# Kernel optimization log

Hardware: AMD Instinct MI355X
Metric: run time of the kernel (lower is better)

## Reference

```python
import jax, jax.numpy as jnp
import numpy as np

N, CH, H, W = 2, 64, 96, 96
NH, CHUNK, RED = 4, 144, 4
CM = CH // RED  # match channels = 16
RES_SCALE = 1.0
NORM_EPS = 5e-5


def conv2d(x, w, b):
    # 3x3 'same' conv, NCHW / OIHW
    y = jax.lax.conv_general_dilated(x, w, (1, 1), 'SAME',
                                     dimension_numbers=('NCHW', 'OIHW', 'NCHW'))
    return y + b[None, :, None, None]


def setup_inputs() -> dict:
    key = jax.random.key(0)
    ks = jax.random.split(key, 8)
    L = H * W
    hb = min(L // CHUNK + (L // CHUNK) % 2, 128)  # = 64
    x = jax.random.normal(ks[0], (N, CH, H, W), jnp.float32)
    # per-round semi-orthogonal rotations: rows of (CM, hb) orthonormal
    g = jax.random.normal(ks[1], (NH, hb, CM), jnp.float32)
    q = jnp.stack([jnp.linalg.qr(g[h])[0] for h in range(NH)])  # (NH, hb, CM)
    rot = jnp.transpose(q, (2, 0, 1))  # (CM, NH, hb)
    def s(k, shape, fan):
        return jax.random.normal(k, shape, jnp.float32) / np.sqrt(fan).astype(np.float32)
    wm = s(ks[2], (CM, CH, 3, 3), CH * 9)
    wa = s(ks[3], (CH, CH, 3, 3), CH * 9)
    wf = s(ks[4], (CH, CH, 3, 3), CH * 9)
    fc1_w = s(ks[5], (CHUNK, CH), CH)
    fc2_w = s(ks[6], (CHUNK, CHUNK), CHUNK)
    return {'x': x, 'rot': rot,
            'wm': wm, 'bm': jnp.zeros((CM,), jnp.float32),
            'wa': wa, 'ba': jnp.zeros((CH,), jnp.float32),
            'wf': wf, 'bf': jnp.zeros((CH,), jnp.float32),
            'fc1_w': fc1_w, 'fc1_b': jnp.zeros((CHUNK,), jnp.float32),
            'fc2_w': fc2_w, 'fc2_b': jnp.zeros((CHUNK,), jnp.float32)}


def reference(x, rot, wm, bm, wa, ba, wf, bf, fc1_w, fc1_b, fc2_w, fc2_b):
    n, _, h, w = x.shape
    L = h * w
    hb = rot.shape[-1]
    # embeddings: (N, L, C)
    xe = jax.nn.relu(conv2d(x, wm, bm)).reshape(n, CM, L).transpose(0, 2, 1)
    ye = jax.nn.relu(conv2d(x, wa, ba)).reshape(n, CH, L).transpose(0, 2, 1)
    fe = jax.nn.relu(conv2d(x, wf, bf)).reshape(n, CH, L).transpose(0, 2, 1)
    # LSH: argmax over rotated directions, offset per round (detached in original)
    rv = jnp.einsum('ntf,fhi->nhti', xe, rot)  # (N, NH, L, hb)
    codes = jnp.argmax(rv, -1) + (jnp.arange(NH) * hb)[None, :, None]
    codes = codes.reshape(n, NH * L)
    idx = jnp.argsort(codes, axis=-1)
    undo = jnp.argsort(idx, axis=-1)
    mod = idx % L
    gather = lambda t: jnp.take_along_axis(t, mod[..., None], axis=1)
    nch = L // CHUNK  # L chosen divisible by CHUNK -> padding = 0
    xs = gather(xe).reshape(n, NH, nch, CHUNK, CM)
    ys = gather(ye).reshape(n, NH, nch, CHUNK, CH)
    fs = gather(fe).reshape(n, NH, nch, CHUNK, CH)
    nrm = jnp.linalg.norm(xs, axis=-1, keepdims=True)
    xmatch = xs / jnp.maximum(nrm, NORM_EPS)
    adj = lambda t: jnp.concatenate([t, jnp.roll(t, 1, axis=2), jnp.roll(t, -1, axis=2)], axis=3)
    xmatch = adj(xmatch)   # (n, NH, nch, 3*CHUNK, CM)
    ya = adj(ys)           # (n, NH, nch, 3*CHUNK, CH)
    fa = adj(fs)           # (n, NH, nch, 3*CHUNK, CH)
    hid = jax.nn.relu(fa @ fc1_w.T + fc1_b)
    fc_raw = jnp.swapaxes(hid @ fc2_w.T + fc2_b, -1, -2)  # (n, NH, nch, CHUNK, 3*CHUNK)
    raw = jnp.einsum('nhkie,nhkje->nhkij', xs, xmatch) + fc_raw
    bsc = jax.scipy.special.logsumexp(raw, axis=-1, keepdims=True)
    score = jnp.exp(raw - bsc)
    ret = jnp.einsum('nhkij,nhkje->nhkie', score, ya)  # (n, NH, nch, CHUNK, CH)
    ret = ret.reshape(n, NH * L, CH)
    bsc = bsc.reshape(n, NH * L)
    ret = jnp.take_along_axis(ret, undo[..., None], axis=1)
    bsc = jnp.take_along_axis(bsc, undo, axis=1)
    ret = ret.reshape(n, NH, L, CH)
    probs = jax.nn.softmax(bsc.reshape(n, NH, L, 1), axis=1)
    out = jnp.sum(ret * probs, axis=1)  # (n, L, CH)
    out = out.transpose(0, 2, 1).reshape(n, CH, h, w)
    return out * RES_SCALE + x
```

## Files before the change

kernel.cpp:

```cpp
#include <hip/hip_runtime.h>
#include <hip/hip_bf16.h>

#define LL 9216
#define TOT 36864
#define CHK 144
#define NSEG 144
#define EPS_N 5e-5f

typedef __bf16 bf16x8 __attribute__((ext_vector_type(8)));
typedef float f32x4 __attribute__((ext_vector_type(4)));

__device__ __forceinline__ float dot4(float4 a, float4 b) {
    return a.x*b.x + a.y*b.y + a.z*b.z + a.w*b.w;
}
__device__ __forceinline__ unsigned short f2bf(float f) {
    __hip_bfloat16 h = __float2bfloat16(f);
    return *reinterpret_cast<unsigned short*>(&h);
}
__device__ __forceinline__ float bf2f(unsigned short u) {
    return __uint_as_float(((unsigned int)u) << 16);
}

__global__ __launch_bounds__(256) void k_front(
    const float* __restrict__ x, const float* __restrict__ wm,
    const float* __restrict__ bm, const float* __restrict__ rot,
    unsigned short* __restrict__ xeb, unsigned short* __restrict__ xnb,
    unsigned char* __restrict__ codes,
    const float* __restrict__ fc1w, const float* __restrict__ fc2w,
    const float* __restrict__ wa, const float* __restrict__ wf,
    unsigned short* __restrict__ w1bf, unsigned short* __restrict__ w2bf,
    unsigned short* __restrict__ wpack)
{
    int tid = threadIdx.x;
    if (blockIdx.x >= 288) {
        int i = (blockIdx.x - 288) * 256 + tid;
        if (i < 144 * 64) w1bf[i] = f2bf(fc1w[i]);
        if (i < 144 * 160) {
            int r = i / 160, c = i - r * 160;
            w2bf[i] = (c < 144) ? f2bf(fc2w[r * 144 + c]) : 0;
        }
        if (i < 128 * 576) {
            int o = i / 576, kk = i - o * 576;
            int dydx = kk >> 6, c = kk & 63;
            const float* src = (o < 64) ? wa : wf;
            wpack[i] = f2bf(src[(o & 63) * 576 + c * 9 + dydx]);
        }
        return;
    }
    __shared__ float xl[6400];
    __shared__ float rotT[4096];
    __shared__ float xsp[64 * 20];
    int b = blockIdx.x;
    int n = b / 144, tile = b % 144;
    int ty0 = (tile / 12) * 8, tx0 = (tile % 12) * 8;
    for (int li = tid; li < 6400; li += 256) {
        int c = li / 100, s = li % 100;
        int yy = s / 10, xx = s % 10;
        int gy = ty0 + yy - 1, gx = tx0 + xx - 1;
        float v = 0.f;
        if ((unsigned)gy < 96u && (unsigned)gx < 96u)
            v = x[((n * 64 + c) * 96 + gy) * 96 + gx];
        xl[li] = v;
    }
    for (int e = tid; e < 4096; e += 256) {
        int f = e >> 8, r = e & 255;
        rotT[r * 16 + f] = rot[f * 256 + r];
    }
    __syncthreads();
    int p = tid & 63, og = tid >> 6;
    int row = p >> 3, col = p & 7;
    int ogs = __builtin_amdgcn_readfirstlane(og);
    const float* wb = wm + (size_t)ogs * 4 * 576;
    float acc0 = 0.f, acc1 = 0.f, acc2 = 0.f, acc3 = 0.f;
    for (int c = 0; c < 64; ++c) {
        float xp[9];
        int base = c * 100 + row * 10 + col;
        #pragma unroll
        for (int dy = 0; dy < 3; ++dy)
            #pragma unroll
            for (int dx = 0; dx < 3; ++dx)
                xp[dy * 3 + dx] = xl[base + dy * 10 + dx];
        const float* w0 = wb + c * 9;
        #pragma unroll
        for (int u = 0; u < 9; ++u) {
            acc0 += w0[u]        * xp[u];
            acc1 += w0[576 + u]  * xp[u];
            acc2 += w0[1152 + u] * xp[u];
            acc3 += w0[1728 + u] * xp[u];
        }
    }
    int o = ogs * 4;
    float v0 = acc0 + bm[o + 0]; v0 = v0 > 0.f ? v0 : 0.f;
    float v1 = acc1 + bm[o + 1]; v1 = v1 > 0.f ? v1 : 0.f;
    float v2 = acc2 + bm[o + 2]; v2 = v2 > 0.f ? v2 : 0.f;
    float v3 = acc3 + bm[o + 3]; v3 = v3 > 0.f ? v3 : 0.f;
    size_t t = (size_t)n * LL + (ty0 + row) * 96 + tx0 + col;
    unsigned short pk[4] = {f2bf(v0), f2bf(v1), f2bf(v2), f2bf(v3)};
    *(uint2*)(xeb + t * 16 + o) = *(uint2*)pk;
    *(float4*)(xsp + p * 20 + o) = make_float4(v0, v1, v2, v3);
    __syncthreads();
    int pos = tid & 63, h = tid >> 6;
    int prow = pos >> 3, pcol = pos & 7;
    size_t tc = (size_t)n * LL + (ty0 + prow) * 96 + tx0 + pcol;
    float4 q0 = *(float4*)(xsp + pos * 20 + 0);
    float4 q1 = *(float4*)(xsp + pos * 20 + 4);
    float4 q2 = *(float4*)(xsp + pos * 20 + 8);
    float4 q3 = *(float4*)(xsp + pos * 20 + 12);
    if (h == 0) {
        float nn = dot4(q0,q0) + dot4(q1,q1) + dot4(q2,q2) + dot4(q3,q3);
        float s = fmaxf(sqrtf(nn), EPS_N);
        float inv = 1.f / s;
        unsigned short pn[16];
        pn[0]=f2bf(q0.x*inv);  pn[1]=f2bf(q0.y*inv);  pn[2]=f2bf(q0.z*inv);  pn[3]=f2bf(q0.w*inv);
        pn[4]=f2bf(q1.x*inv);  pn[5]=f2bf(q1.y*inv);  pn[6]=f2bf(q1.z*inv);  pn[7]=f2bf(q1.w*inv);
        pn[8]=f2bf(q2.x*inv);  pn[9]=f2bf(q2.y*inv);  pn[10]=f2bf(q2.z*inv); pn[11]=f2bf(q2.w*inv);
        pn[12]=f2bf(q3.x*inv); pn[13]=f2bf(q3.y*inv); pn[14]=f2bf(q3.z*inv); pn[15]=f2bf(q3.w*inv);
        *(uint4*)(xnb + tc * 16)     = ((uint4*)pn)[0];
        *(uint4*)(xnb + tc * 16 + 8) = ((uint4*)pn)[1];
    }
    float best = -1e30f; int bi = 0;
    const float* rp = rotT + h * 1024;
    for (int i = 0; i < 64; ++i) {
        const float4* r4 = (const float4*)(rp + i * 16);
        float v = dot4(q0, r4[0]) + dot4(q1, r4[1]) + dot4(q2, r4[2]) + dot4(q3, r4[3]);
        if (v > best) { best = v; bi = i; }
    }
    codes[(size_t)n * TOT + h * LL + (tc - (size_t)n * LL)] = (unsigned char)(h * 64 + bi);
}

__global__ __launch_bounds__(256) void k_convbf_fc(
    const float* __restrict__ x, const unsigned short* __restrict__ wpack,
    const float* __restrict__ ba, const float* __restrict__ bfb,
    const unsigned short* __restrict__ w1bf, const float* __restrict__ fc1_b,
    const unsigned short* __restrict__ w2bf, const float* __restrict__ fc2_b,
    unsigned short* __restrict__ yeb, unsigned short* __restrict__ re2b,
    const unsigned char* __restrict__ codes, int* __restrict__ hist)
{
    __shared__ unsigned short xt[3 * 50 * 72];
    __shared__ unsigned short fet[48 * 72];
    __shared__ unsigned short hb [48 * 168];
    __shared__ int lh[256];
    int tid = threadIdx.x;
    if (blockIdx.x >= 384) {
        int b2 = blockIdx.x - 384;
        int n = b2 / NSEG, seg = b2 % NSEG;
        lh[tid] = 0;
        __syncthreads();
        int code = codes[(size_t)n * TOT + seg * 256 + tid];
        atomicAdd(&lh[code], 1);
        __syncthreads();
        hist[((size_t)n * 256 + tid) * NSEG + seg] = lh[tid];
        return;
    }
    int b = blockIdx.x;
    int n = b / 192, rem = b % 192;
    int y = rem >> 1, strip = rem & 1;
    int x0 = strip * 48;
    for (int e = tid; e < 9600; e += 256) {
        int r = e / 3200, r2 = e - r * 3200;
        int c = r2 / 50, j = r2 - c * 50;
        int gy = y - 1 + r, gx = x0 - 1 + j;
        float v = 0.f;
        if ((unsigned)gy < 96u && (unsigned)gx < 96u)
            v = x[((n * 64 + c) * 96 + gy) * 96 + gx];
        xt[(r * 50 + j) * 72 + c] = f2bf(v);
    }
    for (int e = tid; e < 384; e += 256) {
        int r = e >> 3, pq = e & 7;
        *(unsigned int*)(hb + r * 168 + 144 + pq * 2) = 0;
    }
    __syncthreads();
    int wave = tid >> 6, lane = tid & 63;
    int n16 = lane & 15, quad = lane >> 4;
    f32x4 acc[2][3];
    #pragma unroll
    for (int mi = 0; mi < 2; ++mi)
        #pragma unroll
        for (int nt = 0; nt < 3; ++nt) acc[mi][nt] = (f32x4){0.f, 0.f, 0.f, 0.f};
    #pragma unroll
    for (int s = 0; s < 18; ++s) {
        int dydx = s >> 1, half = s & 1;
        int dy = dydx / 3, dxm = dydx - dy * 3;
        bf16x8 B[3];
        #pragma unroll
        for (int nt = 0; nt < 3; ++nt) {
            int j = nt * 16 + n16 + dxm;
            B[nt] = *(bf16x8*)(xt + (dy * 50 + j) * 72 + half * 32 + quad * 8);
        }
        #pragma unroll
        for (int mi = 0; mi < 2; ++mi) {
            int o = (wave * 2 + mi) * 16 + n16;
            bf16x8 A = *(const bf16x8*)(wpack + o * 576 + dydx * 64 + half * 32 + quad * 8);
            #pragma unroll
            for (int nt = 0; nt < 3; ++nt)
                acc[mi][nt] = __builtin_amdgcn_mfma_f32_16x16x32_bf16(A, B[nt], acc[mi][nt], 0, 0, 0);
        }
    }
    #pragma unroll
    for (int mi = 0; mi < 2; ++mi) {
        int mt = wave * 2 + mi;
        int obase = mt * 16 + quad * 4;
        float4 b4 = (mt < 4) ? *(const float4*)(ba + obase)
                             : *(const float4*)(bfb + obase - 64);
        #pragma unroll
        for (int nt = 0; nt < 3; ++nt) {
            int j = nt * 16 + n16;
            unsigned short pk[4];
            float v0 = acc[mi][nt][0] + b4.x; pk[0] = f2bf(v0 > 0.f ? v0 : 0.f);
            float v1 = acc[mi][nt][1] + b4.y; pk[1] = f2bf(v1 > 0.f ? v1 : 0.f);
            float v2 = acc[mi][nt][2] + b4.z; pk[2] = f2bf(v2 > 0.f ? v2 : 0.f);
            float v3 = acc[mi][nt][3] + b4.w; pk[3] = f2bf(v3 > 0.f ? v3 : 0.f);
            if (mt < 4) {
                size_t t = (size_t)n * LL + y * 96 + x0 + j;
                *(uint2*)(yeb + t * 64 + obase) = *(uint2*)pk;
            } else {
                *(uint2*)(fet + j * 72 + (obase - 64)) = *(uint2*)pk;
            }
        }
    }
    __syncthreads();
    size_t R0 = (size_t)n * LL + y * 96 + x0;
    for (int nt = wave; nt < 9; nt += 4) {
        int bn = nt * 16 + n16;
        bf16x8 b0 = *(const bf16x8*)(w1bf + bn * 64 + quad * 8);
        bf16x8 b1 = *(const bf16x8*)(w1bf + bn * 64 + 32 + quad * 8);
        float bb = fc1_b[bn];
        #pragma unroll
        for (int m = 0; m < 3; ++m) {
            int arow = m * 16 + n16;
            bf16x8 a0 = *(bf16x8*)(fet + arow * 72 + quad * 8);
            bf16x8 a1 = *(bf16x8*)(fet + arow * 72 + 32 + quad * 8);
            f32x4 c2 = {0.f, 0.f, 0.f, 0.f};
            c2 = __builtin_amdgcn_mfma_f32_16x16x32_bf16(a0, b0, c2, 0, 0, 0);
            c2 = __builtin_amdgcn_mfma_f32_16x16x32_bf16(a1, b1, c2, 0, 0, 0);
            #pragma unroll
            for (int r = 0; r < 4; ++r) {
                float v = c2[r] + bb;
                hb[(m * 16 + quad * 4 + r) * 168 + bn] = f2bf(v > 0.f ? v : 0.f);
            }
        }
    }
    __syncthreads();
    for (int nt = wave; nt < 9; nt += 4) {
        int bn = nt * 16 + n16;
        bf16x8 wv2[5];
        #pragma unroll
        for (int kk = 0; kk < 5; ++kk)
            wv2[kk] = *(const bf16x8*)(w2bf + bn * 160 + kk * 32 + quad * 8);
        float bb = fc2_b[bn];
        #pragma unroll
        for (int m = 0; m < 3; ++m) {
            int arow = m * 16 + n16;
            f32x4 c2 = {0.f, 0.f, 0.f, 0.f};
            #pragma unroll
            for (int kk = 0; kk < 5; ++kk) {
                bf16x8 a = *(bf16x8*)(hb + arow * 168 + kk * 32 + quad * 8);
                c2 = __builtin_amdgcn_mfma_f32_16x16x32_bf16(a, wv2[kk], c2, 0, 0, 0);
            }
            #pragma unroll
            for (int r = 0; r < 4; ++r)
                re2b[(R0 + m * 16 + quad * 4 + r) * 144 + bn] = f2bf(c2[r] + bb);
        }
    }
}

__global__ void k_scan(int* __restrict__ hist)
{
    __shared__ int sc[256];
    int n = blockIdx.x, bin = threadIdx.x;
    int* hp = hist + ((size_t)n * 256 + bin) * NSEG;
    int4 buf[36];
    int4* hp4 = (int4*)hp;
    #pragma unroll
    for (int q = 0; q < 36; ++q) buf[q] = hp4[q];
    int running = 0;
    #pragma unroll
    for (int q = 0; q < 36; ++q) {
        int t0 = buf[q].x; buf[q].x = running; running += t0;
        int t1 = buf[q].y; buf[q].y = running; running += t1;
        int t2 = buf[q].z; buf[q].z = running; running += t2;
        int t3 = buf[q].w; buf[q].w = running; running += t3;
    }
    sc[bin] = running;
    __syncthreads();
    for (int off = 1; off < 256; off <<= 1) {
        int v = sc[bin];
        int u = (bin >= off) ? sc[bin - off] : 0;
        __syncthreads();
        sc[bin] = v + u;
        __syncthreads();
    }
    int bs = sc[bin] - running;
    #pragma unroll
    for (int q = 0; q < 36; ++q) {
        buf[q].x += bs; buf[q].y += bs; buf[q].z += bs; buf[q].w += bs;
        hp4[q] = buf[q];
    }
}

__global__ __launch_bounds__(256) void k_place(
    const unsigned char* __restrict__ codes, const int* __restrict__ hist,
    int* __restrict__ idx)
{
    __shared__ unsigned char cl[256];
    int b = blockIdx.x, n = b / NSEG, seg = b % NSEG;
    int tid = threadIdx.x;
    int my = codes[(size_t)n * TOT + seg * 256 + tid];
    cl[tid] = (unsigned char)my;
    __syncthreads();
    int rank = 0;
    for (int j = 0; j < tid; ++j) rank += (cl[j] == my);
    int pos = hist[((size_t)n * 256 + my) * NSEG + seg] + rank;
    idx[(size_t)n * TOT + pos] = seg * 256 + tid;
}

__global__ __launch_bounds__(256) void k_gather(
    const int* __restrict__ idx, const unsigned short* __restrict__ xeb,
    const unsigned short* __restrict__ xnb, const unsigned short* __restrict__ yeb,
    const unsigned short* __restrict__ re2b,
    unsigned short* __restrict__ qs, unsigned short* __restrict__ ks,
    unsigned short* __restrict__ vsT, unsigned short* __restrict__ fst,
    int* __restrict__ undo)
{
    __shared__ int tl[144];
    int b0 = blockIdx.x;
    int b = ((b0 & 7) << 6) | (b0 >> 3);
    int nh = b >> 6, chunk = b & 63;
    int n = nh >> 2, h = nh & 3;
    size_t gb = (size_t)nh * LL + chunk * 144;
    size_t nL = (size_t)n * LL;
    int tid = threadIdx.x;
    if (tid < 144) {
        int t = idx[(size_t)n * TOT + h * LL + chunk * 144 + tid] - h * LL;
        tl[tid] = t;
        undo[(size_t)nh * LL + t] = chunk * 144 + tid;
    }
    __syncthreads();
    for (int e = tid; e < 288; e += 256) {
        int s = e >> 1, half = e & 1;
        size_t src = (nL + tl[s]) * 16 + half * 8;
        *(uint4*)(qs + (gb + s) * 16 + half * 8) = *(const uint4*)(xeb + src);
        *(uint4*)(ks + (gb + s) * 16 + half * 8) = *(const uint4*)(xnb + src);
    }
    size_t vb = (size_t)(nh * 64 + chunk) * 64;
    for (int e = tid; e < 576; e += 256) {
        int p = e % 72, su = e / 72;
        uint4 a  = *(const uint4*)(yeb + (nL + tl[2 * p])     * 64 + su * 8);
        uint4 bq = *(const uint4*)(yeb + (nL + tl[2 * p + 1]) * 64 + su * 8);
        const unsigned short* pa = (const unsigned short*)&a;
        const unsigned short* pb = (const unsigned short*)&bq;
        #pragma unroll
        for (int ci = 0; ci < 8; ++ci) {
            int c = su * 8 + ci;
            *(unsigned int*)(vsT + (vb + c) * 144 + 2 * p) =
                (unsigned int)pa[ci] | ((unsigned int)pb[ci] << 16);
        }
    }
    for (int e = tid; e < 1296; e += 256) {
        int mt = e / 144, s = e - mt * 144;
        const unsigned short* src = re2b + (nL + tl[s]) * 144 + mt * 16;
        unsigned short* dst = fst + ((size_t)(nh * 9 + mt) * LL + chunk * 144 + s) * 16;
        *(uint4*)(dst)     = *(const uint4*)(src);
        *(uint4*)(dst + 8) = *(const uint4*)(src + 8);
    }
}

__global__ __launch_bounds__(256, 2) void k_attn(
    const unsigned short* __restrict__ qs, const unsigned short* __restrict__ ks,
    const unsigned short* __restrict__ vsT, const unsigned short* __restrict__ fst,
    unsigned short* __restrict__ rets, float* __restrict__ bscs)
{
    __shared__ __align__(16) unsigned short Pw[4][16 * 56];

    int B = blockIdx.x;
    int wb = (B & 7) * 144 + (B >> 3);
    int tid = threadIdx.x;
    int lane = tid & 63, wv = tid >> 6;
    int n16 = lane & 15, quad = lane >> 4;
    int job = wb * 4 + wv;
    int bucket = job / 9, mt = job - bucket * 9;
    int n = bucket >> 8, rem = bucket & 255;
    int h = rem >> 6, k = rem & 63;
    int nh = n * 4 + h;

    size_t hL = (size_t)nh * LL;
    int ch0 = k, ch1 = (k + 63) & 63, ch2 = (k + 1) & 63;
    unsigned short* Pp = &Pw[wv][0];
    const unsigned short* fsl = fst + (size_t)(nh * 9 + mt) * LL * 16;

    bf16x8 afragQ = {};
    if (quad < 2)
        afragQ = *(const bf16x8*)(qs + (hL + ch0 * 144 + mt * 16 + n16) * 16 + quad * 8);

    f32x4 acc[4];
    float rm[4], rl[4];
    #pragma unroll
    for (int ct = 0; ct < 4; ++ct) acc[ct] = (f32x4){0.f, 0.f, 0.f, 0.f};
    #pragma unroll
    for (int r = 0; r < 4; ++r) { rm[r] = -1e30f; rl[r] = 0.f; }

#define SLOT(T) ((((T) < 3) ? ch0 : ((T) < 6) ? ch1 : ch2) * 144 + ((T) % 3) * 48)

#define LOAD_KF(T, KS, FV) do {                                                      \
    int sl_ = SLOT(T);                                                               \
    if (quad < 2) {                                                                  \
        KS[0] = *(const bf16x8*)(ks + (hL + sl_ + n16) * 16 + quad * 8);             \
        KS[1] = *(const bf16x8*)(ks + (hL + sl_ + 16 + n16) * 16 + quad * 8);        \
        KS[2] = *(const bf16x8*)(ks + (hL + sl_ + 32 + n16) * 16 + quad * 8);        \
    }                                                                                \
    FV[0] = *(const ushort4*)(fsl + (size_t)(sl_ + n16) * 16 + quad * 4);            \
    FV[1] = *(const ushort4*)(fsl + (size_t)(sl_ + 16 + n16) * 16 + quad * 4);       \
    FV[2] = *(const ushort4*)(fsl + (size_t)(sl_ + 32 + n16) * 16 + quad * 4);       \
} while (0)

#define ATTN_ITER(T, KS, FV, NKS, NFV) do {                                          \
    int chx_ = ((T) < 3) ? ch0 : ((T) < 6) ? ch1 : ch2;                              \
    const unsigned short* vch_ = vsT + (size_t)(nh * 64 + chx_) * 9216;              \
    int vo_ = ((T) % 3) * 48;                                                        \
    bf16x8 Bv0_[4];                                                                  \
    _Pragma("unroll")                                                                \
    for (int ct_ = 0; ct_ < 4; ++ct_)                                                \
        Bv0_[ct_] = *(const bf16x8*)(vch_ + (size_t)(ct_ * 16 + n16) * 144 + vo_ + quad * 8); \
    if ((T) < 8) LOAD_KF((T) + 1, NKS, NFV);                                         \
    f32x4 c0_ = {bf2f(FV[0].x), bf2f(FV[0].y), bf2f(FV[0].z), bf2f(FV[0].w)};        \
    f32x4 c1_ = {bf2f(FV[1].x), bf2f(FV[1].y), bf2f(FV[1].z), bf2f(FV[1].w)};        \
    f32x4 c2_ = {bf2f(FV[2].x), bf2f(FV[2].y), bf2f(FV[2].z), bf2f(FV[2].w)};        \
    c0_ = __builtin_amdgcn_mfma_f32_16x16x32_bf16(afragQ, KS[0], c0_, 0, 0, 0);      \
    c1_ = __builtin_amdgcn_mfma_f32_16x16x32_bf16(afragQ, KS[1], c1_, 0, 0, 0);      \
    c2_ = __builtin_amdgcn_mfma_f32_16x16x32_bf16(afragQ, KS[2], c2_, 0, 0, 0);      \
    _Pragma("unroll")                                                                \
    for (int r_ = 0; r_ < 4; ++r_) {                                                 \
        float v0_ = c0_[r_], v1_ = c1_[r_], v2_ = c2_[r_];                           \
        float mm_ = fmaxf(fmaxf(v0_, v1_), v2_);                                     \
        mm_ = fmaxf(mm_, __shfl_xor(mm_, 1, 16));                                    \
        mm_ = fmaxf(mm_, __shfl_xor(mm_, 2, 16));                                    \
        mm_ = fmaxf(mm_, __shfl_xor(mm_, 4, 16));                                    \
        mm_ = fmaxf(mm_, __shfl_xor(mm_, 8, 16));                                    \
        float mn_ = fmaxf(rm[r_], mm_);                                              \
        float a_ = __expf(rm[r_] - mn_);                                             \
        float s0_ = __expf(v0_ - mn_), s1_ = __expf(v1_ - mn_), s2_ = __expf(v2_ - mn_); \
        float ss_ = s0_ + s1_ + s2_;                                                 \
        ss_ += __shfl_xor(ss_, 1, 16);                                               \
        ss_ += __shfl_xor(ss_, 2, 16);                                               \
        ss_ += __shfl_xor(ss_, 4, 16);                                               \
        ss_ += __shfl_xor(ss_, 8, 16);                                               \
        rl[r_] = rl[r_] * a_ + ss_;                                                  \
        rm[r_] = mn_;                                                                \
        acc[0][r_] *= a_; acc[1][r_] *= a_; acc[2][r_] *= a_; acc[3][r_] *= a_;      \
        int rw_ = quad * 4 + r_;                                                     \
        Pp[rw_ * 56 +      n16] = f2bf(s0_);                                         \
        Pp[rw_ * 56 + 16 + n16] = f2bf(s1_);                                         \
        Pp[rw_ * 56 + 32 + n16] = f2bf(s2_);                                         \
    }                                                                                \
                \
    bf16x8 Ap0_ = *(const bf16x8*)(Pp + n16 * 56 + quad * 8);                        \
    int ko1_ = (quad < 2) ? 32 + quad * 8 : 0;          \
    bf16x8 Bv1_[4];                                                                  \
    _Pragma("unroll")                                                                \
    for (int ct_ = 0; ct_ < 4; ++ct_)                                                \
        Bv1_[ct_] = *(const bf16x8*)(vch_ + (size_t)(ct_ * 16 + n16) * 144 + vo_ + ko1_); \
    _Pragma("unroll")                                                                \
    for (int ct_ = 0; ct_ < 4; ++ct_)                                                \
        acc[ct_] = __builtin_amdgcn_mfma_f32_16x16x32_bf16(Ap0_, Bv0_[ct_], acc[ct_], 0, 0, 0); \
    bf16x8 Ap1_ = {};                                                                \
    if (quad < 2)                                                                    \
        Ap1_ = *(const bf16x8*)(Pp + n16 * 56 + 32 + quad * 8);                      \
    _Pragma("unroll")                                                                \
    for (int ct_ = 0; ct_ < 4; ++ct_)                                                \
        acc[ct_] = __builtin_amdgcn_mfma_f32_16x16x32_bf16(Ap1_, Bv1_[ct_], acc[ct_], 0, 0, 0); \
} while (0)

    bf16x8 ksA[3] = {}, ksB[3] = {};
    ushort4 fvA[3], fvB[3];
    LOAD_KF(0, ksA, fvA);
    ATTN_ITER(0, ksA, fvA, ksB, fvB);
    ATTN_ITER(1, ksB, fvB, ksA, fvA);
    ATTN_ITER(2, ksA, fvA, ksB, fvB);
    ATTN_ITER(3, ksB, fvB, ksA, fvA);
    ATTN_ITER(4, ksA, fvA, ksB, fvB);
    ATTN_ITER(5, ksB, fvB, ksA, fvA);
    ATTN_ITER(6, ksA, fvA, ksB, fvB);
    ATTN_ITER(7, ksB, fvB, ksA, fvA);
    ATTN_ITER(8, ksA, fvA, ksB, fvB);

#undef ATTN_ITER
#undef LOAD_KF
#undef SLOT

    size_t sp0 = hL + ch0 * 144;
    if (n16 == 0) {
        #pragma unroll
        for (int r = 0; r < 4; ++r)
            bscs[sp0 + mt * 16 + quad * 4 + r] = rm[r] + __logf(rl[r]);
    }
    #pragma unroll
    for (int r = 0; r < 4; ++r) {
        float inv = 1.f / rl[r];
        #pragma unroll
        for (int ct = 0; ct < 4; ++ct)
            rets[(sp0 + mt * 16 + quad * 4 + r) * 64 + ct * 16 + n16] =
                f2bf(acc[ct][r] * inv);
    }
}

__global__ __launch_bounds__(256) void k_final(
    const unsigned short* __restrict__ rets, const float* __restrict__ bscs,
    const int* __restrict__ undo, const float* __restrict__ x,
    float* __restrict__ out)
{
    __shared__ float pr[4][64];
    __shared__ int us[4][64];
    __shared__ float accl[64 * 65];
    int b = blockIdx.x, n = b / 144;
    int t0 = (b % 144) * 64;
    int tid = threadIdx.x;
    {
        int h = tid >> 6, tt = tid & 63;
        us[h][tt] = undo[((size_t)n * 4 + h) * LL + t0 + tt];
    }
    __syncthreads();
    if (tid < 64) {
        float b0 = bscs[((size_t)n * 4 + 0) * LL + us[0][tid]];
        float b1 = bscs[((size_t)n * 4 + 1) * LL + us[1][tid]];
        float b2 = bscs[((size_t)n * 4 + 2) * LL + us[2][tid]];
        float b3 = bscs[((size_t)n * 4 + 3) * LL + us[3][tid]];
        float mx = fmaxf(fmaxf(b0, b1), fmaxf(b2, b3));
        float e0 = __expf(b0-mx), e1 = __expf(b1-mx), e2 = __expf(b2-mx), e3 = __expf(b3-mx);
        float inv = 1.f / (e0 + e1 + e2 + e3);
        pr[0][tid] = e0*inv; pr[1][tid] = e1*inv; pr[2][tid] = e2*inv; pr[3][tid] = e3*inv;
    }
    __syncthreads();
    int cc = tid & 63, tt4 = tid >> 6;
    #pragma unroll
    for (int q = 0; q < 16; ++q) {
        int tt = tt4 + 4*q;
        float v = 0.f;
        #pragma unroll
        for (int h2 = 0; h2 < 4; ++h2)
            v += bf2f(rets[(((size_t)n*4 + h2)*LL + us[h2][tt])*64 + cc]) * pr[h2][tt];
        accl[cc*65 + tt] = v;
    }
    __syncthreads();
    int tt = tid & 63, c4 = tid >> 6;
    #pragma unroll
    for (int q = 0; q < 16; ++q) {
        int ch = c4 + 4*q;
        size_t o = ((size_t)n*64 + ch)*LL + t0 + tt;
        out[o] = accl[ch*65 + tt] + x[o];
    }
}

extern "C" void kernel_launch(void* const* d_in, const int* in_sizes, int n_in,
                              void* d_out, int out_size, void* d_ws, size_t ws_size,
                              hipStream_t stream)
{
    const float* x    = (const float*)d_in[0];
    const float* rot  = (const float*)d_in[1];
    const float* wm   = (const float*)d_in[2];
    const float* bm   = (const float*)d_in[3];
    const float* wa   = (const float*)d_in[4];
    const float* ba   = (const float*)d_in[5];
    const float* wf   = (const float*)d_in[6];
    const float* bf   = (const float*)d_in[7];
    const float* fc1w = (const float*)d_in[8];
    const float* fc1b = (const float*)d_in[9];
    const float* fc2w = (const float*)d_in[10];
    const float* fc2b = (const float*)d_in[11];
    float* out = (float*)d_out;

    char* ws = (char*)d_ws;
    unsigned short* xeb  = (unsigned short*)(ws + 0);
    unsigned short* yeb  = (unsigned short*)(ws + 589824);
    unsigned short* xnb  = (unsigned short*)(ws + 2949120);
    unsigned short* re2b = (unsigned short*)(ws + 3538944);
    unsigned short* w1bf = (unsigned short*)(ws + 8847360);
    unsigned short* w2bf = (unsigned short*)(ws + 8865792);
    unsigned short* wpak = (unsigned short*)(ws + 8911872);
    unsigned char* codes = (unsigned char*)(ws + 9059328);
    int* hist            = (int*)(ws + 9133056);
    int* idxb            = (int*)(ws + 9427968);
    unsigned short* rets = (unsigned short*)(ws + 0);
    float* bscs          = (float*)(ws + 9437184);
    unsigned short* qs   = (unsigned short*)(ws + 9732096);
    unsigned short* ks   = (unsigned short*)(ws + 12091392);
    unsigned short* vsT  = (unsigned short*)(ws + 14450688);
    unsigned short* fst  = (unsigned short*)(ws + 23887872);
    int* undo            = (int*)(ws + 45121536);

    k_front    <<<576, 256, 0, stream>>>(x, wm, bm, rot, xeb, xnb, codes,
                                         fc1w, fc2w, wa, wf, w1bf, w2bf, wpak);
    k_convbf_fc<<<672, 256, 0, stream>>>(x, wpak, ba, bf, w1bf, fc1b, w2bf, fc2b,
                                         yeb, re2b, codes, hist);
    k_scan     <<<2,    256, 0, stream>>>(hist);
    k_place    <<<288,  256, 0, stream>>>(codes, hist, idxb);
    k_gather   <<<512,  256, 0, stream>>>(idxb, xeb, xnb, yeb, re2b,
                                          qs, ks, vsT, fst, undo);
    k_attn     <<<1152, 256, 0, stream>>>(qs, ks, vsT, fst, rets, bscs);
    k_final    <<<288,  256, 0, stream>>>(rets, bscs, undo, x, out);
}
```

Before: 225.7 us.

## Restructure front kernels: separate weight prep, co-schedule match conv with main conv

Splits weight conversion into its own small kernel and merges the match-embedding conv/LSH hashing blocks into the same launch as the bf16 MFMA conv+FC blocks, interleaved 3:4 by block index. The histogram moves into its own kernel after the fused launch. The intent is to let the FP32 match conv run concurrently with the heavy MFMA conv instead of serially, at the cost of an extra launch and a larger shared-memory footprint per block, which may reduce occupancy.

```diff
diff --git a/kernel.cpp b/kernel.cpp
--- a/kernel.cpp
+++ b/kernel.cpp
@@ -21,138 +21,128 @@
     return __uint_as_float(((unsigned int)u) << 16);
 }
 
-__global__ __launch_bounds__(256) void k_front(
+__global__ __launch_bounds__(256) void k_wprep(
+    const float* __restrict__ fc1w, const float* __restrict__ fc2w,
+    const float* __restrict__ wa, const float* __restrict__ wf,
+    unsigned short* __restrict__ w1bf, unsigned short* __restrict__ w2bf,
+    unsigned short* __restrict__ wpack)
+{
+    int i = blockIdx.x * 256 + threadIdx.x;
+    if (i < 144 * 64) w1bf[i] = f2bf(fc1w[i]);
+    if (i < 144 * 160) {
+        int r = i / 160, c = i - r * 160;
+        w2bf[i] = (c < 144) ? f2bf(fc2w[r * 144 + c]) : 0;
+    }
+    if (i < 128 * 576) {
+        int o = i / 576, kk = i - o * 576;
+        int dydx = kk >> 6, c = kk & 63;
+        const float* src = (o < 64) ? wa : wf;
+        wpack[i] = f2bf(src[(o & 63) * 576 + c * 9 + dydx]);
+    }
+}
+
+__global__ __launch_bounds__(256) void k_conv2(
     const float* __restrict__ x, const float* __restrict__ wm,
     const float* __restrict__ bm, const float* __restrict__ rot,
     unsigned short* __restrict__ xeb, unsigned short* __restrict__ xnb,
     unsigned char* __restrict__ codes,
-    const float* __restrict__ fc1w, const float* __restrict__ fc2w,
-    const float* __restrict__ wa, const float* __restrict__ wf,
-    unsigned short* __restrict__ w1bf, unsigned short* __restrict__ w2bf,
-    unsigned short* __restrict__ wpack)
-{
-    int tid = threadIdx.x;
-    if (blockIdx.x >= 288) {
-        int i = (blockIdx.x - 288) * 256 + tid;
-        if (i < 144 * 64) w1bf[i] = f2bf(fc1w[i]);
-        if (i < 144 * 160) {
-            int r = i / 160, c = i - r * 160;
-            w2bf[i] = (c < 144) ? f2bf(fc2w[r * 144 + c]) : 0;
-        }
-        if (i < 128 * 576) {
-            int o = i / 576, kk = i - o * 576;
-            int dydx = kk >> 6, c = kk & 63;
-            const float* src = (o < 64) ? wa : wf;
-            wpack[i] = f2bf(src[(o & 63) * 576 + c * 9 + dydx]);
-        }
-        return;
-    }
-    __shared__ float xl[6400];
-    __shared__ float rotT[4096];
-    __shared__ float xsp[64 * 20];
-    int b = blockIdx.x;
-    int n = b / 144, tile = b % 144;
-    int ty0 = (tile / 12) * 8, tx0 = (tile % 12) * 8;
-    for (int li = tid; li < 6400; li += 256) {
-        int c = li / 100, s = li % 100;
-        int yy = s / 10, xx = s % 10;
-        int gy = ty0 + yy - 1, gx = tx0 + xx - 1;
-        float v = 0.f;
-        if ((unsigned)gy < 96u && (unsigned)gx < 96u)
-            v = x[((n * 64 + c) * 96 + gy) * 96 + gx];
-        xl[li] = v;
-    }
-    for (int e = tid; e < 4096; e += 256) {
-        int f = e >> 8, r = e & 255;
-        rotT[r * 16 + f] = rot[f * 256 + r];
-    }
-    __syncthreads();
-    int p = tid & 63, og = tid >> 6;
-    int row = p >> 3, col = p & 7;
-    int ogs = __builtin_amdgcn_readfirstlane(og);
-    const float* wb = wm + (size_t)ogs * 4 * 576;
-    float acc0 = 0.f, acc1 = 0.f, acc2 = 0.f, acc3 = 0.f;
-    for (int c = 0; c < 64; ++c) {
-        float xp[9];
-        int base = c * 100 + row * 10 + col;
-        #pragma unroll
-        for (int dy = 0; dy < 3; ++dy)
-            #pragma unroll
-            for (int dx = 0; dx < 3; ++dx)
-                xp[dy * 3 + dx] = xl[base + dy * 10 + dx];
-        const float* w0 = wb + c * 9;
-        #pragma unroll
-        for (int u = 0; u < 9; ++u) {
-            acc0 += w0[u]        * xp[u];
-            acc1 += w0[576 + u]  * xp[u];
-            acc2 += w0[1152 + u] * xp[u];
-            acc3 += w0[1728 + u] * xp[u];
-        }
-    }
-    int o = ogs * 4;
-    float v0 = acc0 + bm[o + 0]; v0 = v0 > 0.f ? v0 : 0.f;
-    float v1 = acc1 + bm[o + 1]; v1 = v1 > 0.f ? v1 : 0.f;
-    float v2 = acc2 + bm[o + 2]; v2 = v2 > 0.f ? v2 : 0.f;
-    float v3 = acc3 + bm[o + 3]; v3 = v3 > 0.f ? v3 : 0.f;
-    size_t t = (size_t)n * LL + (ty0 + row) * 96 + tx0 + col;
-    unsigned short pk[4] = {f2bf(v0), f2bf(v1), f2bf(v2), f2bf(v3)};
-    *(uint2*)(xeb + t * 16 + o) = *(uint2*)pk;
-    *(float4*)(xsp + p * 20 + o) = make_float4(v0, v1, v2, v3);
-    __syncthreads();
-    int pos = tid & 63, h = tid >> 6;
-    int prow = pos >> 3, pcol = pos & 7;
-    size_t tc = (size_t)n * LL + (ty0 + prow) * 96 + tx0 + pcol;
-    float4 q0 = *(float4*)(xsp + pos * 20 + 0);
-    float4 q1 = *(float4*)(xsp + pos * 20 + 4);
-    float4 q2 = *(float4*)(xsp + pos * 20 + 8);
-    float4 q3 = *(float4*)(xsp + pos * 20 + 12);
-    if (h == 0) {
-        float nn = dot4(q0,q0) + dot4(q1,q1) + dot4(q2,q2) + dot4(q3,q3);
-        float s = fmaxf(sqrtf(nn), EPS_N);
-        float inv = 1.f / s;
-        unsigned short pn[16];
-        pn[0]=f2bf(q0.x*inv);  pn[1]=f2bf(q0.y*inv);  pn[2]=f2bf(q0.z*inv);  pn[3]=f2bf(q0.w*inv);
-        pn[4]=f2bf(q1.x*inv);  pn[5]=f2bf(q1.y*inv);  pn[6]=f2bf(q1.z*inv);  pn[7]=f2bf(q1.w*inv);
-        pn[8]=f2bf(q2.x*inv);  pn[9]=f2bf(q2.y*inv);  pn[10]=f2bf(q2.z*inv); pn[11]=f2bf(q2.w*inv);
-        pn[12]=f2bf(q3.x*inv); pn[13]=f2bf(q3.y*inv); pn[14]=f2bf(q3.z*inv); pn[15]=f2bf(q3.w*inv);
-        *(uint4*)(xnb + tc * 16)     = ((uint4*)pn)[0];
-        *(uint4*)(xnb + tc * 16 + 8) = ((uint4*)pn)[1];
-    }
-    float best = -1e30f; int bi = 0;
-    const float* rp = rotT + h * 1024;
-    for (int i = 0; i < 64; ++i) {
-        const float4* r4 = (const float4*)(rp + i * 16);
-        float v = dot4(q0, r4[0]) + dot4(q1, r4[1]) + dot4(q2, r4[2]) + dot4(q3, r4[3]);
-        if (v > best) { best = v; bi = i; }
-    }
-    codes[(size_t)n * TOT + h * LL + (tc - (size_t)n * LL)] = (unsigned char)(h * 64 + bi);
-}
-
-__global__ __launch_bounds__(256) void k_convbf_fc(
-    const float* __restrict__ x, const unsigned short* __restrict__ wpack,
+    const unsigned short* __restrict__ wpack,
     const float* __restrict__ ba, const float* __restrict__ bfb,
     const unsigned short* __restrict__ w1bf, const float* __restrict__ fc1_b,
     const unsigned short* __restrict__ w2bf, const float* __restrict__ fc2_b,
-    unsigned short* __restrict__ yeb, unsigned short* __restrict__ re2b,
-    const unsigned char* __restrict__ codes, int* __restrict__ hist)
-{
-    __shared__ unsigned short xt[3 * 50 * 72];
-    __shared__ unsigned short fet[48 * 72];
-    __shared__ unsigned short hb [48 * 168];
-    __shared__ int lh[256];
+    unsigned short* __restrict__ yeb, unsigned short* __restrict__ re2b)
+{
+    __shared__ __align__(16) char smem[47104];
     int tid = threadIdx.x;
-    if (blockIdx.x >= 384) {
-        int b2 = blockIdx.x - 384;
-        int n = b2 / NSEG, seg = b2 % NSEG;
-        lh[tid] = 0;
+    int b7 = blockIdx.x % 7, bq = blockIdx.x / 7;
+
+    if (b7 < 3) {
+        float* xl   = (float*)smem;
+        float* rotT = (float*)(smem + 25600);
+        float* xsp  = (float*)(smem + 41984);
+        int b = bq * 3 + b7;
+        int n = b / 144, tile = b % 144;
+        int ty0 = (tile / 12) * 8, tx0 = (tile % 12) * 8;
+        for (int li = tid; li < 6400; li += 256) {
+            int c = li / 100, s = li % 100;
+            int yy = s / 10, xx = s % 10;
+            int gy = ty0 + yy - 1, gx = tx0 + xx - 1;
+            float v = 0.f;
+            if ((unsigned)gy < 96u && (unsigned)gx < 96u)
+                v = x[((n * 64 + c) * 96 + gy) * 96 + gx];
+            xl[li] = v;
+        }
+        for (int e = tid; e < 4096; e += 256) {
+            int f = e >> 8, r = e & 255;
+            rotT[r * 16 + f] = rot[f * 256 + r];
+        }
         __syncthreads();
-        int code = codes[(size_t)n * TOT + seg * 256 + tid];
-        atomicAdd(&lh[code], 1);
+        int p = tid & 63, og = tid >> 6;
+        int row = p >> 3, col = p & 7;
+        int ogs = __builtin_amdgcn_readfirstlane(og);
+        const float* wb = wm + (size_t)ogs * 4 * 576;
+        float acc0 = 0.f, acc1 = 0.f, acc2 = 0.f, acc3 = 0.f;
+        for (int c = 0; c < 64; ++c) {
+            float xp[9];
+            int base = c * 100 + row * 10 + col;
+            #pragma unroll
+            for (int dy = 0; dy < 3; ++dy)
+                #pragma unroll
+                for (int dx = 0; dx < 3; ++dx)
+                    xp[dy * 3 + dx] = xl[base + dy * 10 + dx];
+            const float* w0 = wb + c * 9;
+            #pragma unroll
+            for (int u = 0; u < 9; ++u) {
+                acc0 += w0[u]        * xp[u];
+                acc1 += w0[576 + u]  * xp[u];
+                acc2 += w0[1152 + u] * xp[u];
+                acc3 += w0[1728 + u] * xp[u];
+            }
+        }
+        int o = ogs * 4;
+        float v0 = acc0 + bm[o + 0]; v0 = v0 > 0.f ? v0 : 0.f;
+        float v1 = acc1 + bm[o + 1]; v1 = v1 > 0.f ? v1 : 0.f;
+        float v2 = acc2 + bm[o + 2]; v2 = v2 > 0.f ? v2 : 0.f;
+        float v3 = acc3 + bm[o + 3]; v3 = v3 > 0.f ? v3 : 0.f;
+        size_t t = (size_t)n * LL + (ty0 + row) * 96 + tx0 + col;
+        unsigned short pk[4] = {f2bf(v0), f2bf(v1), f2bf(v2), f2bf(v3)};
+        *(uint2*)(xeb + t * 16 + o) = *(uint2*)pk;
+        *(float4*)(xsp + p * 20 + o) = make_float4(v0, v1, v2, v3);
         __syncthreads();
-        hist[((size_t)n * 256 + tid) * NSEG + seg] = lh[tid];
+        int pos = tid & 63, h = tid >> 6;
+        int prow = pos >> 3, pcol = pos & 7;
+        size_t tc = (size_t)n * LL + (ty0 + prow) * 96 + tx0 + pcol;
+        float4 q0 = *(float4*)(xsp + pos * 20 + 0);
+        float4 q1 = *(float4*)(xsp + pos * 20 + 4);
+        float4 q2 = *(float4*)(xsp + pos * 20 + 8);
+        float4 q3 = *(float4*)(xsp + pos * 20 + 12);
+        if (h == 0) {
+            float nn = dot4(q0,q0) + dot4(q1,q1) + dot4(q2,q2) + dot4(q3,q3);
+            float s = fmaxf(sqrtf(nn), EPS_N);
+            float inv = 1.f / s;
+            unsigned short pn[16];
+            pn[0]=f2bf(q0.x*inv);  pn[1]=f2bf(q0.y*inv);  pn[2]=f2bf(q0.z*inv);  pn[3]=f2bf(q0.w*inv);
+            pn[4]=f2bf(q1.x*inv);  pn[5]=f2bf(q1.y*inv);  pn[6]=f2bf(q1.z*inv);  pn[7]=f2bf(q1.w*inv);
+            pn[8]=f2bf(q2.x*inv);  pn[9]=f2bf(q2.y*inv);  pn[10]=f2bf(q2.z*inv); pn[11]=f2bf(q2.w*inv);
+            pn[12]=f2bf(q3.x*inv); pn[13]=f2bf(q3.y*inv); pn[14]=f2bf(q3.z*inv); pn[15]=f2bf(q3.w*inv);
+            *(uint4*)(xnb + tc * 16)     = ((uint4*)pn)[0];
+            *(uint4*)(xnb + tc * 16 + 8) = ((uint4*)pn)[1];
+        }
+        float best = -1e30f; int bi = 0;
+        const float* rp = rotT + h * 1024;
+        for (int i = 0; i < 64; ++i) {
+            const float4* r4 = (const float4*)(rp + i * 16);
+            float v = dot4(q0, r4[0]) + dot4(q1, r4[1]) + dot4(q2, r4[2]) + dot4(q3, r4[3]);
+            if (v > best) { best = v; bi = i; }
+        }
+        codes[(size_t)n * TOT + h * LL + (tc - (size_t)n * LL)] = (unsigned char)(h * 64 + bi);
         return;
     }
-    int b = blockIdx.x;
+
+    unsigned short* xt  = (unsigned short*)smem;
+    unsigned short* fet = (unsigned short*)(smem + 21600);
+    unsigned short* hb  = (unsigned short*)(smem + 28512);
+    int b = bq * 4 + (b7 - 3);
     int n = b / 192, rem = b % 192;
     int y = rem >> 1, strip = rem & 1;
     int x0 = strip * 48;
@@ -262,6 +252,21 @@
                 re2b[(R0 + m * 16 + quad * 4 + r) * 144 + bn] = f2bf(c2[r] + bb);
         }
     }
+}
+
+__global__ __launch_bounds__(256) void k_hist(
+    const unsigned char* __restrict__ codes, int* __restrict__ hist)
+{
+    __shared__ int lh[256];
+    int b2 = blockIdx.x;
+    int n = b2 / NSEG, seg = b2 % NSEG;
+    int tid = threadIdx.x;
+    lh[tid] = 0;
+    __syncthreads();
+    int code = codes[(size_t)n * TOT + seg * 256 + tid];
+    atomicAdd(&lh[code], 1);
+    __syncthreads();
+    hist[((size_t)n * 256 + tid) * NSEG + seg] = lh[tid];
 }
 
 __global__ void k_scan(int* __restrict__ hist)
@@ -587,10 +592,11 @@
     unsigned short* fst  = (unsigned short*)(ws + 23887872);
     int* undo            = (int*)(ws + 45121536);
 
-    k_front    <<<576, 256, 0, stream>>>(x, wm, bm, rot, xeb, xnb, codes,
-                                         fc1w, fc2w, wa, wf, w1bf, w2bf, wpak);
-    k_convbf_fc<<<672, 256, 0, stream>>>(x, wpak, ba, bf, w1bf, fc1b, w2bf, fc2b,
-                                         yeb, re2b, codes, hist);
+    k_wprep    <<<288,  256, 0, stream>>>(fc1w, fc2w, wa, wf, w1bf, w2bf, wpak);
+    k_conv2    <<<672,  256, 0, stream>>>(x, wm, bm, rot, xeb, xnb, codes,
+                                          wpak, ba, bf, w1bf, fc1b, w2bf, fc2b,
+                                          yeb, re2b);
+    k_hist     <<<288,  256, 0, stream>>>(codes, hist);
     k_scan     <<<2,    256, 0, stream>>>(hist);
     k_place    <<<288,  256, 0, stream>>>(codes, hist, idxb);
     k_gather   <<<512,  256, 0, stream>>>(idxb, xeb, xnb, yeb, re2b,
```

Result: faster. 201.9 us (-10.5%).
